# Performance work log

Measured on AMD Instinct MI355X. Metric: run time of the kernel, lower is better.

The kernel has to match this reference:

```python
import jax, jax.numpy as jnp
import numpy as np

N_NODES = 50000
N_EDGES = 400000
D = 300          # num_features == hidden_units
L = 5            # num_layers
C = 128          # num_outputs
NG = 256         # graphs per batch
BN_EPS = 1e-5


def setup_inputs() -> dict:
    key = jax.random.key(0)
    ks = jax.random.split(key, 16)
    x = jax.random.normal(ks[0], (N_NODES, D), dtype=jnp.float32)
    edge_index = jax.random.randint(ks[1], (2, N_EDGES), 0, N_NODES, dtype=jnp.int64)
    batch = jnp.sort(jax.random.randint(ks[2], (N_NODES,), 0, NG, dtype=jnp.int64))
    s = 1.0 / np.sqrt(D)
    # Stacked per-layer GINConv MLP params: Linear -> BN -> ReLU -> Linear, then outer BN
    mlp_W1 = jax.random.uniform(ks[3], (L, D, D), jnp.float32, -s, s)
    mlp_b1 = jax.random.uniform(ks[4], (L, D), jnp.float32, -s, s)
    mlp_g1 = jnp.ones((L, D), jnp.float32)
    mlp_be1 = jnp.zeros((L, D), jnp.float32)
    mlp_W2 = jax.random.uniform(ks[5], (L, D, D), jnp.float32, -s, s)
    mlp_b2 = jax.random.uniform(ks[6], (L, D), jnp.float32, -s, s)
    bn_g = jnp.ones((L, D), jnp.float32)
    bn_b = jnp.zeros((L, D), jnp.float32)
    # num_layers+1 readout heads (num_features == hidden_units so all [D, C])
    fc_W = jax.random.uniform(ks[7], (L + 1, D, C), jnp.float32, -s, s)
    fc_b = jax.random.uniform(ks[8], (L + 1, C), jnp.float32, -s, s)
    return dict(x=x, edge_index=edge_index, batch=batch,
                mlp_W1=mlp_W1, mlp_b1=mlp_b1, mlp_g1=mlp_g1, mlp_be1=mlp_be1,
                mlp_W2=mlp_W2, mlp_b2=mlp_b2, bn_g=bn_g, bn_b=bn_b,
                fc_W=fc_W, fc_b=fc_b)


def _bn(h, gamma, beta):
    # BatchNorm1d in training mode: biased batch stats over the node dim
    mu = h.mean(axis=0)
    var = h.var(axis=0)
    return (h - mu) * jax.lax.rsqrt(var + BN_EPS) * gamma + beta


def reference(x, edge_index, batch, mlp_W1, mlp_b1, mlp_g1, mlp_be1,
              mlp_W2, mlp_b2, bn_g, bn_b, fc_W, fc_b):
    src, dst = edge_index[0], edge_index[1]
    n = x.shape[0]
    outs = [x]
    h = x
    for i in range(L):
        # GINConv (eps=0): MLP(x + sum_{j in N(i)} x_j), scatter-add over edges
        agg = jax.ops.segment_sum(h[src], dst, num_segments=n)
        z = h + agg
        z = z @ mlp_W1[i] + mlp_b1[i]
        z = jax.nn.relu(_bn(z, mlp_g1[i], mlp_be1[i]))
        z = z @ mlp_W2[i] + mlp_b2[i]
        h = jax.nn.relu(_bn(z, bn_g[i], bn_b[i]))  # outer BN + ReLU
        outs.append(h)
    # global mean pool per graph, then per-depth linear heads summed (dropout off in eval)
    counts = jax.ops.segment_sum(jnp.ones((n,), x.dtype), batch, num_segments=NG)
    inv = 1.0 / jnp.maximum(counts, 1.0)
    out = jnp.zeros((NG, C), x.dtype)
    for i, hi in enumerate(outs):
        pooled = jax.ops.segment_sum(hi, batch, num_segments=NG) * inv[:, None]
        out = out + (pooled @ fc_W[i] + fc_b[i])
    return out
```

## Files before the change

### kernel.cpp

```cpp
#include <hip/hip_runtime.h>

#define D 300
#define KP 320
#define NPAD 50048
#define NT128 391
#define TPB 2
#define GB 196
#define WSTRIDE 328
#define NGR 256
#define NL 5
#define NC 128
#define BN_EPS 1e-5f

typedef __attribute__((ext_vector_type(8))) short bf16x8;
typedef __attribute__((ext_vector_type(4))) float f32x4;
typedef unsigned short u16;

__device__ __forceinline__ void atomAdd(float* p, float v) { unsafeAtomicAdd(p, v); }

__device__ __forceinline__ short f2bf(float f) {
    union { float f; unsigned u; } v; v.f = f;
    unsigned r = v.u + 0x7fffu + ((v.u >> 16) & 1u);
    return (short)(r >> 16);
}
__device__ __forceinline__ float bf2f(short s) {
    union { unsigned u; float f; } v;
    v.u = ((unsigned)(u16)s) << 16;
    return v.f;
}
__device__ __forceinline__ unsigned cvtpk(float lo, float hi) {
    unsigned r;
    asm("v_cvt_pk_bf16_f32 %0, %1, %2" : "=v"(r) : "v"(lo), "v"(hi));
    return r;
}

__global__ void offsets_kernel(const int* __restrict__ batch, int* __restrict__ off, int N) {
    int g = threadIdx.x;
    if (g > NGR) return;
    int lo = 0, hi = N;
    while (lo < hi) {
        int mid = (lo + hi) >> 1;
        if (batch[mid] < g) lo = mid + 1; else hi = mid;
    }
    off[g] = lo;
}

__global__ __launch_bounds__(256)
void deg_kernel(const int* __restrict__ ei, int* __restrict__ deg, int E) {
    int e = blockIdx.x * 256 + threadIdx.x;
    if (e < E) atomicAdd(&deg[ei[E + e]], 1);
}

__global__ __launch_bounds__(256)
void degpart_kernel(const int* __restrict__ deg, int* __restrict__ part, int N) {
    int i = blockIdx.x * 256 + threadIdx.x;
    int v = (i < N) ? deg[i] : 0;
    #pragma unroll
    for (int o = 1; o < 64; o <<= 1) v += __shfl_xor(v, o);
    __shared__ int ws[4];
    if ((threadIdx.x & 63) == 0) ws[threadIdx.x >> 6] = v;
    __syncthreads();
    if (threadIdx.x == 0) part[blockIdx.x] = ws[0] + ws[1] + ws[2] + ws[3];
}

__global__ __launch_bounds__(256)
void partscan_kernel(int* __restrict__ part, int nb) {
    __shared__ int buf[256];
    int t = threadIdx.x;
    int v = (t < nb) ? part[t] : 0;
    buf[t] = v;
    __syncthreads();
    for (int o = 1; o < 256; o <<= 1) {
        int u = (t >= o) ? buf[t - o] : 0;
        __syncthreads();
        buf[t] += u;
        __syncthreads();
    }
    if (t < nb) part[t] = (t == 0) ? 0 : buf[t - 1];
}

__global__ __launch_bounds__(256)
void rowptr_kernel(const int* __restrict__ deg, const int* __restrict__ part,
                   int* __restrict__ rowptr, int N, int E) {
    __shared__ int buf[256];
    int b = blockIdx.x, t = threadIdx.x;
    int i = b * 256 + t;
    int v = (i < N) ? deg[i] : 0;
    buf[t] = v;
    __syncthreads();
    for (int o = 1; o < 256; o <<= 1) {
        int u = (t >= o) ? buf[t - o] : 0;
        __syncthreads();
        buf[t] += u;
        __syncthreads();
    }
    if (i < N) rowptr[i] = part[b] + buf[t] - v;
    if (b == 0 && t == 0) rowptr[N] = E;
}

__global__ __launch_bounds__(256)
void fill_kernel(const int* __restrict__ ei, const int* __restrict__ rowptr,
                 int* __restrict__ cursor, int* __restrict__ col, int E) {
    int e = blockIdx.x * 256 + threadIdx.x;
    if (e >= E) return;
    int src = ei[e];
    int dst = ei[E + e];
    int pos = atomicAdd(&cursor[dst], 1);
    col[rowptr[dst] + pos] = src;
}

__global__ __launch_bounds__(256)
void wcvt_kernel(const float* __restrict__ W1, const float* __restrict__ W2,
                 u16* __restrict__ Wt) {
    int idx = blockIdx.x * 256 + threadIdx.x;
    if (idx >= 10 * KP * 80) return;
    int n4 = idx % 80;
    int k = (idx / 80) % KP;
    int mat = idx / (80 * KP);
    const float* Wsrc = (mat < NL) ? (W1 + (size_t)mat * D * D) : (W2 + (size_t)(mat - NL) * D * D);
    float4 w = make_float4(0.f, 0.f, 0.f, 0.f);
    if (k < D && n4 < 75) w = *(const float4*)(Wsrc + (size_t)k * D + n4 * 4);
    size_t base = ((size_t)mat * 320 + n4 * 4) * KP + k;
    Wt[base]          = (u16)f2bf(w.x);
    Wt[base + KP]     = (u16)f2bf(w.y);
    Wt[base + 2 * KP] = (u16)f2bf(w.z);
    Wt[base + 3 * KP] = (u16)f2bf(w.w);
}

__global__ __launch_bounds__(256)
void xcvt_kernel(const float* __restrict__ x, u16* __restrict__ xbf, int N) {
    int idx = blockIdx.x * 256 + threadIdx.x;
    if (idx >= NPAD * 40) return;
    int row = idx / 40;
    int c8 = (idx - row * 40) * 8;
    short o[8];
    #pragma unroll
    for (int i = 0; i < 8; ++i) {
        int c = c8 + i;
        float f = (row < N && c < D) ? x[(size_t)row * D + c] : 0.f;
        o[i] = f2bf(f);
    }
    *(bf16x8*)(xbf + (size_t)row * KP + c8) = *(bf16x8*)o;
}

template<bool APPLY>
__global__ __launch_bounds__(256)
void gather_kernel(const u16* __restrict__ H, u16* __restrict__ Z,
                   const int* __restrict__ rowptr, const int* __restrict__ col,
                   const float* __restrict__ scsh, int N) {
    int idx = blockIdx.x * 256 + threadIdx.x;
    if (idx >= N * 40) return;
    int node = idx / 40;
    int c8 = (idx - node * 40) * 8;
    float sc[8], sh[8];
    if (APPLY) {
        #pragma unroll
        for (int i = 0; i < 8; ++i) { sc[i] = scsh[c8 + i]; sh[i] = scsh[KP + c8 + i]; }
    }
    int s = rowptr[node], e = rowptr[node + 1];
    bf16x8 v = *(const bf16x8*)(H + (size_t)node * KP + c8);
    float acc[8];
    #pragma unroll
    for (int i = 0; i < 8; ++i) {
        float f = bf2f(v[i]);
        acc[i] = APPLY ? fmaxf(fmaf(f, sc[i], sh[i]), 0.f) : f;
    }
    int j = s;
    for (; j + 2 <= e; j += 2) {
        int s0 = col[j], s1 = col[j + 1];
        bf16x8 w0 = *(const bf16x8*)(H + (size_t)s0 * KP + c8);
        bf16x8 w1 = *(const bf16x8*)(H + (size_t)s1 * KP + c8);
        #pragma unroll
        for (int i = 0; i < 8; ++i) {
            float f0 = bf2f(w0[i]);
            float f1 = bf2f(w1[i]);
            acc[i] += APPLY ? fmaxf(fmaf(f0, sc[i], sh[i]), 0.f) : f0;
            acc[i] += APPLY ? fmaxf(fmaf(f1, sc[i], sh[i]), 0.f) : f1;
        }
    }
    if (j < e) {
        int s0 = col[j];
        bf16x8 w0 = *(const bf16x8*)(H + (size_t)s0 * KP + c8);
        #pragma unroll
        for (int i = 0; i < 8; ++i) {
            float f0 = bf2f(w0[i]);
            acc[i] += APPLY ? fmaxf(fmaf(f0, sc[i], sh[i]), 0.f) : f0;
        }
    }
    short o[8];
    #pragma unroll
    for (int i = 0; i < 8; ++i) o[i] = f2bf(acc[i]);
    *(bf16x8*)(Z + (size_t)node * KP + c8) = *(bf16x8*)o;
}

template<bool APPLY>
__global__ __launch_bounds__(320)
void pool_kernel(const u16* __restrict__ H, const int* __restrict__ off,
                 const float* __restrict__ scsh, float* __restrict__ pooled_l) {
    __shared__ float red[8][KP];
    int t = threadIdx.x;
    int g = blockIdx.x;
    int rq = t / 40;
    int c8 = (t - rq * 40) * 8;
    float sc[8], sh[8];
    if (APPLY) {
        #pragma unroll
        for (int i = 0; i < 8; ++i) { sc[i] = scsh[c8 + i]; sh[i] = scsh[KP + c8 + i]; }
    }
    int r0 = off[g], r1 = off[g + 1];
    float a[8] = {};
    for (int r = r0 + rq; r < r1; r += 8) {
        bf16x8 v = *(const bf16x8*)(H + (size_t)r * KP + c8);
        #pragma unroll
        for (int i = 0; i < 8; ++i) {
            float f = bf2f(v[i]);
            a[i] += APPLY ? fmaxf(fmaf(f, sc[i], sh[i]), 0.f) : f;
        }
    }
    #pragma unroll
    for (int i = 0; i < 8; ++i) red[rq][c8 + i] = a[i];
    __syncthreads();
    int c = t;
    if (c < D) {
        float s = 0.f;
        #pragma unroll
        for (int j = 0; j < 8; ++j) s += red[j][c];
        pooled_l[g * D + c] = s;
    }
}

template<bool APPLY>
__global__ __launch_bounds__(256, 3)
void mfma_gemm_kernel(const u16* __restrict__ Abf, const u16* __restrict__ Wt,
                      const float* __restrict__ bias, const float* __restrict__ scsh,
                      u16* __restrict__ Cbf, float* __restrict__ stats, int Nreal) {
    __shared__ u16 Ws[80 * WSTRIDE];
    __shared__ float lsum[80], lsq[80];
    const int tid = threadIdx.x;
    const int nBase = blockIdx.y * 80;
    const int wave = tid >> 6, lane = tid & 63;
    const int quad = lane >> 4, l16 = lane & 15;

    const int tile0 = blockIdx.x * TPB;
    const u16* pA = Abf + (size_t)(tile0 * 128 + wave * 16 + l16) * KP + quad * 8;
    bf16x8 a[2][10];
    #pragma unroll
    for (int kc = 0; kc < 10; ++kc) {
        a[0][kc] = *(const bf16x8*)(pA + kc * 32);
        a[1][kc] = *(const bf16x8*)(pA + (size_t)64 * KP + kc * 32);
    }

    {
        const u16* src = Wt + (size_t)nBase * KP;
        for (int unit = tid; unit < 80 * 40; unit += 256) {
            int n = unit / 40, kg = unit - n * 40;
            *(bf16x8*)&Ws[n * WSTRIDE + kg * 8] =
                *(const bf16x8*)(src + (size_t)n * KP + kg * 8);
        }
    }
    if (tid < 80) { lsum[tid] = 0.f; lsq[tid] = 0.f; }
    __syncthreads();

    const size_t adv = (tile0 + 1 < NT128) ? (size_t)128 * KP : 0;

    #pragma unroll
    for (int t = 0; t < TPB; ++t) {
        const int tile = tile0 + t;

        if (APPLY) {
            #pragma unroll
            for (int kc = 0; kc < 10; ++kc) {
                const float* sp = scsh + kc * 32 + quad * 8;
                float4 s0 = *(const float4*)sp;
                float4 s1 = *(const float4*)(sp + 4);
                float4 h0 = *(const float4*)(sp + KP);
                float4 h1 = *(const float4*)(sp + KP + 4);
                float sc[8] = {s0.x, s0.y, s0.z, s0.w, s1.x, s1.y, s1.z, s1.w};
                float sh[8] = {h0.x, h0.y, h0.z, h0.w, h1.x, h1.y, h1.z, h1.w};
                #pragma unroll
                for (int g = 0; g < 2; ++g) {
                    float f[8];
                    #pragma unroll
                    for (int i = 0; i < 8; ++i)
                        f[i] = fmaxf(fmaf(bf2f(a[g][kc][i]), sc[i], sh[i]), 0.f);
                    union { unsigned u[4]; bf16x8 v; } o;
                    o.u[0] = cvtpk(f[0], f[1]);
                    o.u[1] = cvtpk(f[2], f[3]);
                    o.u[2] = cvtpk(f[4], f[5]);
                    o.u[3] = cvtpk(f[6], f[7]);
                    a[g][kc] = o.v;
                }
            }
        }

        f32x4 acc[2][5] = {};
        #pragma unroll
        for (int kc = 0; kc < 10; ++kc) {
            #pragma unroll
            for (int nt = 0; nt < 5; ++nt) {
                bf16x8 b = *(const bf16x8*)&Ws[(nt * 16 + l16) * WSTRIDE + kc * 32 + quad * 8];
                acc[0][nt] = __builtin_amdgcn_mfma_f32_16x16x32_bf16(a[0][kc], b, acc[0][nt], 0, 0, 0);
                acc[1][nt] = __builtin_amdgcn_mfma_f32_16x16x32_bf16(a[1][kc], b, acc[1][nt], 0, 0, 0);
            }
            if (t == 0) {
                a[0][kc] = *(const bf16x8*)(pA + adv + kc * 32);
                a[1][kc] = *(const bf16x8*)(pA + adv + (size_t)64 * KP + kc * 32);
            }
        }

        if (tile < NT128) {
            const int rb = tile * 128 + wave * 16 + quad * 4;
            #pragma unroll
            for (int nt = 0; nt < 5; ++nt) {
                const int nl = nt * 16 + l16;
                const int colg = nBase + nl;
                if (colg < D) {
                    const float bia = bias[colg];
                    float s = 0.f, q = 0.f;
                    #pragma unroll
                    for (int g = 0; g < 2; ++g) {
                        const int rg = rb + g * 64;
                        #pragma unroll
                        for (int rp = 0; rp < 2; ++rp) {
                            const int row0 = rg + rp * 2;
                            float v0 = acc[g][nt][rp * 2]     + bia;
                            float v1 = acc[g][nt][rp * 2 + 1] + bia;
                            if (row0 >= Nreal)     v0 = 0.f;
                            if (row0 + 1 >= Nreal) v1 = 0.f;
                            s += v0 + v1;
                            q = fmaf(v0, v0, fmaf(v1, v1, q));
                            const unsigned pk = cvtpk(v0, v1);
                            Cbf[(size_t)row0 * KP + colg]       = (u16)(pk & 0xffffu);
                            Cbf[(size_t)(row0 + 1) * KP + colg] = (u16)(pk >> 16);
                        }
                    }
                    s += __shfl_xor(s, 16); s += __shfl_xor(s, 32);
                    q += __shfl_xor(q, 16); q += __shfl_xor(q, 32);
                    if (quad == 0) { atomicAdd(&lsum[nl], s); atomicAdd(&lsq[nl], q); }
                }
            }
        }
    }
    __syncthreads();
    if (tid < 80) {
        int colg = nBase + tid;
        if (colg < D) {
            atomAdd(&stats[colg], lsum[tid]);
            atomAdd(&stats[KP + colg], lsq[tid]);
        }
    }
}

__global__ void bnfin_kernel(float* __restrict__ sums, const float* __restrict__ g,
                             const float* __restrict__ be, float* __restrict__ scsh, float invN) {
    int c = threadIdx.x;
    if (c >= D) return;
    float mu = sums[c] * invN;
    float var = sums[KP + c] * invN - mu * mu;
    float s = g[c] / sqrtf(var + BN_EPS);
    scsh[c] = s;
    scsh[KP + c] = fmaf(-mu, s, be[c]);
    sums[c] = 0.f;
    sums[KP + c] = 0.f;
}

__global__ __launch_bounds__(128)
void bias_init_kernel(const float* __restrict__ fcb, float* __restrict__ out) {
    int i = blockIdx.x * 128 + threadIdx.x;
    if (i >= NGR * NC) return;
    int c = i & (NC - 1);
    float s = 0.f;
    for (int l = 0; l <= NL; ++l) s += fcb[l * NC + c];
    out[i] = s;
}

__global__ __launch_bounds__(128)
void readout_kernel(const float* __restrict__ pooled, const int* __restrict__ off,
                    const float* __restrict__ fcW, float* __restrict__ out) {
    __shared__ float sp[4][D];
    int c = threadIdx.x;
    int l = blockIdx.y;
    int g0 = blockIdx.x * 4;
    for (int i = c; i < 4 * D; i += 128) {
        int gg = i / D, k = i - gg * D;
        sp[gg][k] = pooled[((size_t)l * NGR + g0 + gg) * D + k];
    }
    __syncthreads();
    float acc[4] = {0.f, 0.f, 0.f, 0.f};
    for (int k = 0; k < D; ++k) {
        float w = fcW[((size_t)l * D + k) * NC + c];
        #pragma unroll
        for (int gg = 0; gg < 4; ++gg) acc[gg] = fmaf(sp[gg][k], w, acc[gg]);
    }
    #pragma unroll
    for (int gg = 0; gg < 4; ++gg) {
        int g = g0 + gg;
        float inv = 1.0f / fmaxf((float)(off[g + 1] - off[g]), 1.0f);
        atomAdd(&out[g * NC + c], acc[gg] * inv);
    }
}

extern "C" void kernel_launch(void* const* d_in, const int* in_sizes, int n_in,
                              void* d_out, int out_size, void* d_ws, size_t ws_size,
                              hipStream_t stream) {
    const float* x       = (const float*)d_in[0];
    const int*   ei      = (const int*)d_in[1];
    const int*   batch   = (const int*)d_in[2];
    const float* W1  = (const float*)d_in[3];
    const float* b1  = (const float*)d_in[4];
    const float* g1  = (const float*)d_in[5];
    const float* be1 = (const float*)d_in[6];
    const float* W2  = (const float*)d_in[7];
    const float* b2  = (const float*)d_in[8];
    const float* bng = (const float*)d_in[9];
    const float* bnb = (const float*)d_in[10];
    const float* fcW = (const float*)d_in[11];
    const float* fcb = (const float*)d_in[12];
    float* out = (float*)d_out;

    const int N = in_sizes[0] / D;
    const int E = in_sizes[1] / 2;
    const int nb = (N + 255) / 256;

    u16* xbf  = (u16*)d_ws;
    u16* bufA = xbf + (size_t)NPAD * KP;
    u16* bufB = bufA + (size_t)NPAD * KP;
    u16* Wt   = bufB + (size_t)NPAD * KP;
    float* pooled = (float*)(Wt + (size_t)10 * 320 * KP);
    float* stats  = pooled + (size_t)(NL + 1) * NGR * D;
    float* sc1    = stats + 2 * KP;
    float* sc2    = sc1 + 2 * KP;
    int*   off    = (int*)(sc2 + 2 * KP);
    int*   rowptr = off + NGR + 1;
    int*   cursor = rowptr + N + 1;
    int*   col    = cursor + N;
    int*   part   = col + E;

    hipMemsetAsync(stats, 0, 6 * KP * sizeof(float), stream);
    offsets_kernel<<<1, 320, 0, stream>>>(batch, off, N);
    bias_init_kernel<<<(NGR * NC + 127) / 128, 128, 0, stream>>>(fcb, out);

    hipMemsetAsync(cursor, 0, N * sizeof(int), stream);
    deg_kernel<<<(E + 255) / 256, 256, 0, stream>>>(ei, cursor, E);
    degpart_kernel<<<nb, 256, 0, stream>>>(cursor, part, N);
    partscan_kernel<<<1, 256, 0, stream>>>(part, nb);
    rowptr_kernel<<<nb, 256, 0, stream>>>(cursor, part, rowptr, N, E);
    hipMemsetAsync(cursor, 0, N * sizeof(int), stream);
    fill_kernel<<<(E + 255) / 256, 256, 0, stream>>>(ei, rowptr, cursor, col, E);

    wcvt_kernel<<<(10 * KP * 80 + 255) / 256, 256, 0, stream>>>(W1, W2, Wt);
    xcvt_kernel<<<(NPAD * 40 + 255) / 256, 256, 0, stream>>>(x, xbf, N);

    const dim3 gemm_grid(GB, 4);
    const int nd40 = N * 40;
    float invN = 1.0f / (float)N;
    const size_t WtM = (size_t)320 * KP;

    pool_kernel<false><<<NGR, 320, 0, stream>>>(xbf, off, sc2, pooled);

    u16* g = bufA;
    u16* t = bufB;
    const u16* src = xbf;
    for (int l = 0; l < NL; ++l) {
        if (l == 0)
            gather_kernel<false><<<(nd40 + 255) / 256, 256, 0, stream>>>(src, g, rowptr, col, sc2, N);
        else
            gather_kernel<true><<<(nd40 + 255) / 256, 256, 0, stream>>>(src, g, rowptr, col, sc2, N);
        mfma_gemm_kernel<false><<<gemm_grid, 256, 0, stream>>>(
            g, Wt + (size_t)l * WtM, b1 + l * D, sc1, t, stats, N);
        bnfin_kernel<<<1, 320, 0, stream>>>(stats, g1 + l * D, be1 + l * D, sc1, invN);
        mfma_gemm_kernel<true><<<gemm_grid, 256, 0, stream>>>(
            t, Wt + (size_t)(NL + l) * WtM, b2 + l * D, sc1, g, stats, N);
        bnfin_kernel<<<1, 320, 0, stream>>>(stats, bng + l * D, bnb + l * D, sc2, invN);
        pool_kernel<true><<<NGR, 320, 0, stream>>>(g, off, sc2, pooled + (size_t)(l + 1) * NGR * D);
        src = g;
        u16* tmp = g; g = t; t = tmp;
    }
    readout_kernel<<<dim3(NGR / 4, NL + 1), 128, 0, stream>>>(pooled, off, fcW, out);
}
```

Baseline: 1.038 ms.

## Swizzle weight LDS layout, transpose MFMA operands for vectorized stores, DPP stat reduction

Stores the weight tile in LDS with an XOR swizzle on the k-quad to avoid bank conflicts, and swaps the MFMA A/B operands so each lane holds four consecutive output columns of one row. The epilogue can then write packed 8-byte bf16 stores and load bias as float4, instead of scattered 2-byte stores. Column BN statistics are reduced with DPP row-shift adds over 16 lanes instead of cross-quad shuffles. It also adds sched_group_barrier hints and s_setprio around the MFMA loop. The trade-off is more per-element reductions (four columns per lane) and some masking logic. Rows past Nreal are now written with the bias value rather than zero, though they are still excluded from the statistics.

New measurement: 1.011 ms. 1.03x faster.

```diff
diff --git a/kernel.cpp b/kernel.cpp
--- a/kernel.cpp
+++ b/kernel.cpp
@@ -32,6 +32,18 @@
     unsigned r;
     asm("v_cvt_pk_bf16_f32 %0, %1, %2" : "=v"(r) : "v"(lo), "v"(hi));
     return r;
+}
+template<int C>
+__device__ __forceinline__ float rs_add(float v) {
+    int x = __builtin_amdgcn_update_dpp(0, __float_as_int(v), C, 0xF, 0xF, true);
+    return v + __int_as_float(x);
+}
+__device__ __forceinline__ float red16(float v) {
+    v = rs_add<0x111>(v);
+    v = rs_add<0x112>(v);
+    v = rs_add<0x114>(v);
+    v = rs_add<0x118>(v);
+    return v;
 }
 
 __global__ void offsets_kernel(const int* __restrict__ batch, int* __restrict__ off, int N) {
@@ -249,17 +261,24 @@
         a[0][kc] = *(const bf16x8*)(pA + kc * 32);
         a[1][kc] = *(const bf16x8*)(pA + (size_t)64 * KP + kc * 32);
     }
+    __builtin_amdgcn_sched_group_barrier(0x020, 20, 0);
 
     {
         const u16* src = Wt + (size_t)nBase * KP;
         for (int unit = tid; unit < 80 * 40; unit += 256) {
             int n = unit / 40, kg = unit - n * 40;
-            *(bf16x8*)&Ws[n * WSTRIDE + kg * 8] =
+            int kc = kg >> 2, q = kg & 3;
+            *(bf16x8*)&Ws[n * WSTRIDE + kc * 32 + ((q ^ (n & 3)) << 3)] =
                 *(const bf16x8*)(src + (size_t)n * KP + kg * 8);
         }
     }
     if (tid < 80) { lsum[tid] = 0.f; lsq[tid] = 0.f; }
     __syncthreads();
+
+    int wb[5];
+    #pragma unroll
+    for (int nt = 0; nt < 5; ++nt)
+        wb[nt] = (nt * 16 + l16) * WSTRIDE + ((quad ^ (l16 & 3)) << 3);
 
     const size_t adv = (tile0 + 1 < NT128) ? (size_t)128 * KP : 0;
 
@@ -294,49 +313,68 @@
         }
 
         f32x4 acc[2][5] = {};
+        __builtin_amdgcn_s_setprio(1);
         #pragma unroll
         for (int kc = 0; kc < 10; ++kc) {
             #pragma unroll
             for (int nt = 0; nt < 5; ++nt) {
-                bf16x8 b = *(const bf16x8*)&Ws[(nt * 16 + l16) * WSTRIDE + kc * 32 + quad * 8];
-                acc[0][nt] = __builtin_amdgcn_mfma_f32_16x16x32_bf16(a[0][kc], b, acc[0][nt], 0, 0, 0);
-                acc[1][nt] = __builtin_amdgcn_mfma_f32_16x16x32_bf16(a[1][kc], b, acc[1][nt], 0, 0, 0);
+                bf16x8 b = *(const bf16x8*)&Ws[wb[nt] + kc * 32];
+                acc[0][nt] = __builtin_amdgcn_mfma_f32_16x16x32_bf16(b, a[0][kc], acc[0][nt], 0, 0, 0);
+                acc[1][nt] = __builtin_amdgcn_mfma_f32_16x16x32_bf16(b, a[1][kc], acc[1][nt], 0, 0, 0);
             }
             if (t == 0) {
                 a[0][kc] = *(const bf16x8*)(pA + adv + kc * 32);
                 a[1][kc] = *(const bf16x8*)(pA + adv + (size_t)64 * KP + kc * 32);
             }
-        }
+            __builtin_amdgcn_sched_group_barrier(0x100, 5, 0);
+            __builtin_amdgcn_sched_group_barrier(0x008, 10, 0);
+            if (t == 0)
+                __builtin_amdgcn_sched_group_barrier(0x020, 2, 0);
+        }
+        __builtin_amdgcn_s_setprio(0);
 
         if (tile < NT128) {
-            const int rb = tile * 128 + wave * 16 + quad * 4;
+            const int r0g = tile * 128 + wave * 16 + l16;
+            const bool ok0 = r0g < Nreal, ok1 = (r0g + 64) < Nreal;
+            u16* crow0 = Cbf + (size_t)r0g * KP + nBase + quad * 4;
+            u16* crow1 = crow0 + (size_t)64 * KP;
             #pragma unroll
             for (int nt = 0; nt < 5; ++nt) {
-                const int nl = nt * 16 + l16;
-                const int colg = nBase + nl;
-                if (colg < D) {
-                    const float bia = bias[colg];
-                    float s = 0.f, q = 0.f;
+                const int c0 = nBase + nt * 16 + quad * 4;
+                float bia[4], msk[4];
+                if (c0 + 3 < D) {
+                    float4 b4 = *(const float4*)(bias + c0);
+                    bia[0] = b4.x; bia[1] = b4.y; bia[2] = b4.z; bia[3] = b4.w;
+                    msk[0] = msk[1] = msk[2] = msk[3] = 1.f;
+                } else {
                     #pragma unroll
-                    for (int g = 0; g < 2; ++g) {
-                        const int rg = rb + g * 64;
-                        #pragma unroll
-                        for (int rp = 0; rp < 2; ++rp) {
-                            const int row0 = rg + rp * 2;
-                            float v0 = acc[g][nt][rp * 2]     + bia;
-                            float v1 = acc[g][nt][rp * 2 + 1] + bia;
-                            if (row0 >= Nreal)     v0 = 0.f;
-                            if (row0 + 1 >= Nreal) v1 = 0.f;
-                            s += v0 + v1;
-                            q = fmaf(v0, v0, fmaf(v1, v1, q));
-                            const unsigned pk = cvtpk(v0, v1);
-                            Cbf[(size_t)row0 * KP + colg]       = (u16)(pk & 0xffffu);
-                            Cbf[(size_t)(row0 + 1) * KP + colg] = (u16)(pk >> 16);
-                        }
+                    for (int r = 0; r < 4; ++r) {
+                        bool vld = (c0 + r) < D;
+                        msk[r] = vld ? 1.f : 0.f;
+                        bia[r] = vld ? bias[c0 + r] : 0.f;
                     }
-                    s += __shfl_xor(s, 16); s += __shfl_xor(s, 32);
-                    q += __shfl_xor(q, 16); q += __shfl_xor(q, 32);
-                    if (quad == 0) { atomicAdd(&lsum[nl], s); atomicAdd(&lsq[nl], q); }
+                }
+                float v0[4], v1[4];
+                #pragma unroll
+                for (int r = 0; r < 4; ++r) {
+                    v0[r] = (acc[0][nt][r] + bia[r]) * msk[r];
+                    v1[r] = (acc[1][nt][r] + bia[r]) * msk[r];
+                }
+                uint2 w0, w1;
+                w0.x = cvtpk(v0[0], v0[1]); w0.y = cvtpk(v0[2], v0[3]);
+                w1.x = cvtpk(v1[0], v1[1]); w1.y = cvtpk(v1[2], v1[3]);
+                *(uint2*)(crow0 + nt * 16) = w0;
+                *(uint2*)(crow1 + nt * 16) = w1;
+                #pragma unroll
+                for (int r = 0; r < 4; ++r) {
+                    float s0 = ok0 ? v0[r] : 0.f;
+                    float s1 = ok1 ? v1[r] : 0.f;
+                    float sv = red16(s0 + s1);
+                    float qv = red16(fmaf(s0, s0, s1 * s1));
+                    if (l16 == 15) {
+                        atomicAdd(&lsum[nt * 16 + quad * 4 + r], sv);
+                        atomicAdd(&lsq [nt * 16 + quad * 4 + r], qv);
+                    }
                 }
             }
         }
```
